# Kernel optimization log

Measured on AMD Instinct MI355X. Metric: run time of the kernel, lower is better.

## Reference

```python
import jax, jax.numpy as jnp
import numpy as np

N = 100_000      # total nodes
E = 1_600_000    # directed edges (before self loops)
G = 1024         # graphs in batch
HEADS, HID, EMB, NCLS = 4, 32, 32, 2
SLOPE = 0.2      # GATConv leaky_relu negative slope
BN_EPS = 1e-5


def setup_inputs() -> dict:
    key = jax.random.key(0)
    ks = jax.random.split(key, 20)
    s = 0.1
    return {
        "x": jax.random.normal(ks[0], (N, 2), jnp.float32),
        "edge_index": jax.random.randint(ks[1], (2, E), 0, N, dtype=jnp.int32),
        "batch": jnp.sort(jax.random.randint(ks[2], (N,), 0, G, dtype=jnp.int32)),
        "W1": jax.random.normal(ks[3], (2, HEADS * HID), jnp.float32) * s,
        "as1": jax.random.normal(ks[4], (HEADS, HID), jnp.float32) * s,
        "ad1": jax.random.normal(ks[5], (HEADS, HID), jnp.float32) * s,
        "b1": jnp.zeros((HEADS * HID,), jnp.float32),
        "g1": jnp.ones((HEADS * HID,), jnp.float32),
        "be1": jnp.zeros((HEADS * HID,), jnp.float32),
        # --- GAT layer 2: 128 -> 32, 1 head, no concat ---
        "W2": jax.random.normal(ks[6], (HEADS * HID, EMB), jnp.float32) * s,
        "as2": jax.random.normal(ks[7], (1, EMB), jnp.float32) * s,
        "ad2": jax.random.normal(ks[8], (1, EMB), jnp.float32) * s,
        "b2": jnp.zeros((EMB,), jnp.float32),
        "g2": jnp.ones((EMB,), jnp.float32),
        "be2": jnp.zeros((EMB,), jnp.float32),
        # --- classifier ---
        "Wc": jax.random.normal(ks[9], (EMB, NCLS), jnp.float32) * s,
        "bc": jnp.zeros((NCLS,), jnp.float32),
    }


def gat_conv(x, src, dst, W, a_src, a_dst, bias, concat):
    """PyG-style GATConv (self loops already appended to src/dst)."""
    n = x.shape[0]
    heads, out = a_src.shape
    h = (x @ W).reshape(n, heads, out)                     # [N,H,D]
    al_src = jnp.sum(h * a_src[None], -1)                  # [N,H]
    al_dst = jnp.sum(h * a_dst[None], -1)                  # [N,H]
    e = jax.nn.leaky_relu(al_src[src] + al_dst[dst], SLOPE)  # [E',H]
    # segment softmax over edges sharing a destination (self loops guarantee coverage)
    m = jax.ops.segment_max(e, dst, num_segments=n)
    e = jnp.exp(e - m[dst])
    z = jax.ops.segment_sum(e, dst, num_segments=n)
    alpha = e / (z[dst] + 1e-16)                           # [E',H]
    msg = h[src] * alpha[:, :, None]                       # [E',H,D]
    out_nodes = jax.ops.segment_sum(msg, dst, num_segments=n)  # [N,H,D]
    if concat:
        return out_nodes.reshape(n, heads * out) + bias
    return out_nodes.mean(1) + bias


def batch_norm(x, gamma, beta):
    mu = x.mean(0)
    var = x.var(0)
    return (x - mu) * jax.lax.rsqrt(var + BN_EPS) * gamma + beta


def reference(x, edge_index, batch, W1, as1, ad1, b1, g1, be1,
              W2, as2, ad2, b2, g2, be2, Wc, bc):
    n = x.shape[0]
    loop = jnp.arange(n, dtype=edge_index.dtype)
    src = jnp.concatenate([edge_index[0], loop])
    dst = jnp.concatenate([edge_index[1], loop])

    h = gat_conv(x, src, dst, W1, as1, ad1, b1, concat=True)
    h = jax.nn.elu(batch_norm(h, g1, be1))     # dropout: eval mode (identity)
    h = gat_conv(h, src, dst, W2, as2, ad2, b2, concat=False)
    h = jax.nn.elu(batch_norm(h, g2, be2))

    # global mean pool per graph
    sums = jax.ops.segment_sum(h, batch, num_segments=G)
    cnt = jax.ops.segment_sum(jnp.ones((n,), h.dtype), batch, num_segments=G)
    emb = sums / jnp.maximum(cnt, 1.0)[:, None]            # [G,EMB]
    return emb @ Wc + bc                                   # [G,2]
```

## Files before the change

kernel.cpp:

```cpp
#include <hip/hip_runtime.h>
#include <hip/hip_bf16.h>
#include <math.h>

#define HEADS 4
#define HID 32
#define EMB 32
#define SLOPE 0.2f
#define BN_EPS 1e-5f
#define STATS_BLOCKS 256
#define MB 128
#define BNUM 256
#define P 256

typedef __attribute__((ext_vector_type(8))) short short8;
typedef __attribute__((ext_vector_type(4))) float fx4;

__device__ __forceinline__ float lrelu(float x) { return x > 0.f ? x : SLOPE * x; }
__device__ __forceinline__ float elu(float x) { return x > 0.f ? x : expm1f(x); }

__device__ __forceinline__ unsigned f2bf_pack(float a, float b) {
    unsigned ua = __float_as_uint(a);
    unsigned ub = __float_as_uint(b);
    unsigned ra = (ua + 0x7fffu + ((ua >> 16) & 1u)) >> 16;
    unsigned rb = (ub + 0x7fffu + ((ub >> 16) & 1u)) >> 16;
    return ra | (rb << 16);
}
__device__ __forceinline__ float bf_lo(unsigned p) { return __uint_as_float(p << 16); }
__device__ __forceinline__ float bf_hi(unsigned p) { return __uint_as_float(p & 0xffff0000u); }

union BfFrag { unsigned u[4]; short8 v; };

__global__ void k_prep(const float* __restrict__ W1, const float* __restrict__ as1,
                       const float* __restrict__ ad1, float* __restrict__ MsMd) {
    int t = threadIdx.x;
    if (t >= 16) return;
    int r = (t >> 2) & 1, h = t & 3;
    const float* a = (t >= 8) ? ad1 : as1;
    float s = 0.f;
#pragma unroll
    for (int d = 0; d < 32; d++) s += W1[r * 128 + h * 32 + d] * a[h * 32 + d];
    MsMd[t] = s;
}

__global__ void __launch_bounds__(256) k_hist(const int* __restrict__ ei,
                                              int* __restrict__ ghist, int E_, int CH) {
    __shared__ int h[BNUM];
    int t = threadIdx.x, p = blockIdx.x;
    h[t] = 0;
    __syncthreads();
    int beg = p * CH, end = beg + CH;
    if (end > E_) end = E_;
    for (int e = beg + t; e < end; e += 256) atomicAdd(&h[ei[E_ + e] >> 9], 1);
    __syncthreads();
    ghist[p * BNUM + t] = h[t];
}

__global__ void __launch_bounds__(1024) k_gscan(const int* __restrict__ ghist,
                                                int* __restrict__ goff, int* __restrict__ sbase,
                                                int* __restrict__ rp, int N_, int E_) {
    __shared__ int s[1024];
    int t = threadIdx.x;
    const int PER = (BNUM * P) / 1024;
    int b0 = t >> 2;
    int p0 = (t & 3) * PER;
    int v[PER];
    int sum = 0;
#pragma unroll
    for (int k = 0; k < PER; k++) {
        v[k] = ghist[(p0 + k) * BNUM + b0];
        sum += v[k];
    }
    s[t] = sum;
    __syncthreads();
    for (int off = 1; off < 1024; off <<= 1) {
        int a = (t >= off) ? s[t - off] : 0;
        __syncthreads();
        s[t] += a;
        __syncthreads();
    }
    int run = s[t] - sum;
#pragma unroll
    for (int k = 0; k < PER; k++) {
        if (p0 + k == 0) sbase[b0] = run;
        goff[(p0 + k) * BNUM + b0] = run;
        run += v[k];
    }
    if (t == 0) {
        sbase[BNUM] = E_;
        rp[N_] = E_ + N_;
    }
}

__global__ void __launch_bounds__(256) k_scatter3(const int* __restrict__ ei,
                                                  const int* __restrict__ goff,
                                                  unsigned* __restrict__ staged,
                                                  int E_, int CH) {
    __shared__ int loff[BNUM];
    __shared__ int lpos[BNUM];
    int t = threadIdx.x, p = blockIdx.x;
    loff[t] = goff[p * BNUM + t];
    lpos[t] = 0;
    __syncthreads();
    int beg = p * CH, end = beg + CH;
    if (end > E_) end = E_;
    for (int e = beg + t; e < end; e += 256) {
        int s = ei[e], d = ei[E_ + e];
        int b = d >> 9;
        unsigned pk = ((unsigned)s << 9) | (unsigned)(d & 511);
        int pos = loff[b] + atomicAdd(&lpos[b], 1);
        staged[pos] = pk;
    }
}

__global__ void __launch_bounds__(512) k_bucket(const unsigned* __restrict__ staged,
                                                const int* __restrict__ sbase,
                                                int* __restrict__ rp, int* __restrict__ esrc,
                                                int N_) {
    int b = blockIdx.x;
    int n0 = b << 9;
    int nn = N_ - n0;
    if (nn > 512) nn = 512;
    if (nn <= 0) return;
    __shared__ int lc[512];
    __shared__ int sc[512];
    __shared__ int wpos[512];
    int t = threadIdx.x;
    lc[t] = 0;
    __syncthreads();
    int sb = sbase[b];
    int m = sbase[b + 1] - sb;
    int eb = sb + (b << 9);
    for (int i = t; i < m; i += 512) atomicAdd(&lc[staged[sb + i] & 511], 1);
    __syncthreads();
    sc[t] = lc[t];
    __syncthreads();
    for (int off = 1; off < 512; off <<= 1) {
        int a = (t >= off) ? sc[t - off] : 0;
        __syncthreads();
        sc[t] += a;
        __syncthreads();
    }
    if (t < nn) {
        int r = eb + (sc[t] - lc[t]) + t;
        rp[n0 + t] = r;
        wpos[t] = r;
        esrc[r + lc[t]] = n0 + t;
    }
    __syncthreads();
    for (int i = t; i < m; i += 512) {
        unsigned p = staged[sb + i];
        int q = atomicAdd(&wpos[p & 511], 1);
        esrc[q] = (int)(p >> 9);
    }
}

__global__ void __launch_bounds__(256) k_agg1f(
        const float* __restrict__ x, const int* __restrict__ rp,
        const int* __restrict__ esrc, const float* __restrict__ MsMd,
        float* __restrict__ nsum, int n) {
    __shared__ float sM[16];
    int t = threadIdx.x;
    if (t < 16) sM[t] = MsMd[t];
    __syncthreads();
    int node = blockIdx.x * 64 + (t >> 2);
    int h = t & 3;
    if (node >= n) return;
    int beg = rp[node], end = rp[node + 1];
    const float2 xd = *reinterpret_cast<const float2*>(&x[(size_t)node * 2]);
    float ald = xd.x * sM[8 + h] + xd.y * sM[12 + h];
    float ms0 = sM[h], ms1 = sM[4 + h];
    float z = 0.f, sx = 0.f, sy = 0.f;
#pragma unroll 2
    for (int e = beg; e < end; e++) {
        int s = esrc[e];
        float2 xs = *reinterpret_cast<const float2*>(&x[(size_t)s * 2]);
        float al = xs.x * ms0 + xs.y * ms1;
        float w = __expf(lrelu(al + ald));
        z += w;
        sx = fmaf(w, xs.x, sx);
        sy = fmaf(w, xs.y, sy);
    }
    float inv = 1.f / (z + 1e-16f);
    nsum[(size_t)node * 8 + h] = sx * inv;
    nsum[(size_t)node * 8 + 4 + h] = sy * inv;
}

__global__ void __launch_bounds__(256) k_mstats(const float* __restrict__ nsum,
                                                float* __restrict__ mpart, int n) {
    int t = threadIdx.x;
    float m[20];
#pragma unroll
    for (int j = 0; j < 20; j++) m[j] = 0.f;
    for (int node = blockIdx.x * 256 + t; node < n; node += gridDim.x * 256) {
        float4 a = *reinterpret_cast<const float4*>(&nsum[(size_t)node * 8]);
        float4 b = *reinterpret_cast<const float4*>(&nsum[(size_t)node * 8 + 4]);
        m[0] += a.x; m[1] += b.x; m[2] += a.x * a.x; m[3] += b.x * b.x; m[4] += a.x * b.x;
        m[5] += a.y; m[6] += b.y; m[7] += a.y * a.y; m[8] += b.y * b.y; m[9] += a.y * b.y;
        m[10] += a.z; m[11] += b.z; m[12] += a.z * a.z; m[13] += b.z * b.z; m[14] += a.z * b.z;
        m[15] += a.w; m[16] += b.w; m[17] += a.w * a.w; m[18] += b.w * b.w; m[19] += a.w * b.w;
    }
#pragma unroll
    for (int off = 1; off < 64; off <<= 1)
#pragma unroll
        for (int j = 0; j < 20; j++) m[j] += __shfl_xor(m[j], off);
    __shared__ float ls[4][20];
    if ((t & 63) == 0)
#pragma unroll
        for (int j = 0; j < 20; j++) ls[t >> 6][j] = m[j];
    __syncthreads();
    if (t < 20) mpart[blockIdx.x * 20 + t] = ls[0][t] + ls[1][t] + ls[2][t] + ls[3][t];
}

__global__ void k_bn1fin(const float* __restrict__ mpart, const float* __restrict__ W1,
                         const float* __restrict__ b1, const float* __restrict__ g1,
                         const float* __restrict__ be1, float4* __restrict__ PQR,
                         int n, int nb) {
    int c = threadIdx.x;
    if (c >= 128) return;
    int h = c >> 5;
    float mx = 0.f, my = 0.f, mxx = 0.f, myy = 0.f, mxy = 0.f;
    for (int b = 0; b < nb; b++) {
        const float* p = &mpart[b * 20 + h * 5];
        mx += p[0]; my += p[1]; mxx += p[2]; myy += p[3]; mxy += p[4];
    }
    float invn = 1.f / (float)n;
    mx *= invn; my *= invn; mxx *= invn; myy *= invn; mxy *= invn;
    float w0 = W1[c], w1 = W1[128 + c], bb = b1[c];
    float mu = w0 * mx + w1 * my + bb;
    float ex2 = w0 * w0 * mxx + w1 * w1 * myy + 2.f * w0 * w1 * mxy
              + 2.f * bb * (w0 * mx + w1 * my) + bb * bb;
    float var = ex2 - mu * mu;
    float A = g1[c] * rsqrtf(var + BN_EPS);
    float B = be1[c] - mu * A;
    PQR[c] = make_float4(A * w0, A * w1, A * bb + B, 0.f);
}

__global__ void __launch_bounds__(256) k_node2m(
        const float* __restrict__ nsum, const float4* __restrict__ PQR,
        const float* __restrict__ W2, const float* __restrict__ as2,
        const float* __restrict__ ad2, unsigned* __restrict__ h2bf,
        float* __restrict__ als2, float* __restrict__ ald2, int n) {
    int t = threadIdx.x;
    int wave = t >> 6, lane = t & 63;
    int col = lane & 15;
    int kgrp = lane >> 4;
    int nb = blockIdx.x * 64 + wave * 16;
    if (nb >= n) return;
    int nodeA = nb + col;
    float4 sx4 = make_float4(0.f, 0.f, 0.f, 0.f), sy4 = sx4;
    if (nodeA < n) {
        sx4 = *reinterpret_cast<const float4*>(&nsum[(size_t)nodeA * 8]);
        sy4 = *reinterpret_cast<const float4*>(&nsum[(size_t)nodeA * 8 + 4]);
    }
    BfFrag b1f[4], b2f[4];
#pragma unroll
    for (int kblk = 0; kblk < 4; kblk++) {
#pragma unroll
        for (int j = 0; j < 8; j += 2) {
            int k = kblk * 32 + kgrp * 8 + j;
            b1f[kblk].u[j >> 1] = f2bf_pack(W2[k * 32 + col], W2[(k + 1) * 32 + col]);
            b2f[kblk].u[j >> 1] = f2bf_pack(W2[k * 32 + 16 + col], W2[(k + 1) * 32 + 16 + col]);
        }
    }
    fx4 acc1 = {0.f, 0.f, 0.f, 0.f};
    fx4 acc2 = {0.f, 0.f, 0.f, 0.f};
    float sxh, syh;
#pragma unroll
    for (int kblk = 0; kblk < 4; kblk++) {
        if (kblk == 0) { sxh = sx4.x; syh = sy4.x; }
        else if (kblk == 1) { sxh = sx4.y; syh = sy4.y; }
        else if (kblk == 2) { sxh = sx4.z; syh = sy4.z; }
        else { sxh = sx4.w; syh = sy4.w; }
        BfFrag af;
        float yk[8];
#pragma unroll
        for (int j = 0; j < 8; j++) {
            int k = kblk * 32 + kgrp * 8 + j;
            float4 pqr = PQR[k];
            yk[j] = elu(fmaf(pqr.x, sxh, fmaf(pqr.y, syh, pqr.z)));
        }
#pragma unroll
        for (int j = 0; j < 8; j += 2) af.u[j >> 1] = f2bf_pack(yk[j], yk[j + 1]);
        acc1 = __builtin_amdgcn_mfma_f32_16x16x32_bf16(af.v, b1f[kblk].v, acc1, 0, 0, 0);
        acc2 = __builtin_amdgcn_mfma_f32_16x16x32_bf16(af.v, b2f[kblk].v, acc2, 0, 0, 0);
    }
    float a2c = as2[col], a2c2 = as2[16 + col];
    float d2c = ad2[col], d2c2 = ad2[16 + col];
#pragma unroll
    for (int r = 0; r < 4; r++) {
        int node = nb + kgrp * 4 + r;
        float v1 = acc1[r], v2 = acc2[r];
        float pS = v1 * a2c + v2 * a2c2;
        float pD = v1 * d2c + v2 * d2c2;
#pragma unroll
        for (int off = 1; off < 16; off <<= 1) {
            pS += __shfl_xor(pS, off);
            pD += __shfl_xor(pD, off);
        }
        float v1n = __shfl_xor(v1, 1);
        float v2n = __shfl_xor(v2, 1);
        if (node < n) {
            if ((col & 1) == 0) {
                h2bf[(size_t)node * 16 + (col >> 1)] = f2bf_pack(v1, v1n);
                h2bf[(size_t)node * 16 + 8 + (col >> 1)] = f2bf_pack(v2, v2n);
            }
            if (col == 0) { als2[node] = pS; ald2[node] = pD; }
        }
    }
}

__global__ void k_stats(const float* __restrict__ x, float* __restrict__ partials,
                        int n, int C) {
    int t = threadIdx.x;
    int G4 = C >> 2;
    int c4 = t & (G4 - 1);
    int rr = t / G4;
    int RPB = 256 / G4;
    float sx = 0.f, sy = 0.f, sz = 0.f, sw_ = 0.f;
    float qx = 0.f, qy = 0.f, qz = 0.f, qw = 0.f;
    for (int r = blockIdx.x * RPB + rr; r < n; r += gridDim.x * RPB) {
        float4 v = *reinterpret_cast<const float4*>(&x[(size_t)r * C + 4 * c4]);
        sx += v.x; sy += v.y; sz += v.z; sw_ += v.w;
        qx += v.x * v.x; qy += v.y * v.y; qz += v.z * v.z; qw += v.w * v.w;
    }
    __shared__ float4 ls[256], ls2[256];
    ls[t] = make_float4(sx, sy, sz, sw_);
    ls2[t] = make_float4(qx, qy, qz, qw);
    __syncthreads();
    if (rr == 0) {
        for (int j = 1; j < RPB; j++) {
            float4 a = ls[j * G4 + c4], b = ls2[j * G4 + c4];
            sx += a.x; sy += a.y; sz += a.z; sw_ += a.w;
            qx += b.x; qy += b.y; qz += b.z; qw += b.w;
        }
        *reinterpret_cast<float4*>(&partials[(size_t)blockIdx.x * 2 * C + 4 * c4]) =
            make_float4(sx, sy, sz, sw_);
        *reinterpret_cast<float4*>(&partials[(size_t)blockIdx.x * 2 * C + C + 4 * c4]) =
            make_float4(qx, qy, qz, qw);
    }
}
__global__ void k_stats2(const float* __restrict__ partials, const float* __restrict__ gamma,
                         const float* __restrict__ beta, float* __restrict__ AB,
                         int n, int C, int nb) {
    __shared__ float ls[512], ls2[512];
    int t = threadIdx.x;
    int R = 512 / C;
    int c = t & (C - 1);
    int r = t / C;
    float s = 0.f, s2 = 0.f;
    for (int b = r; b < nb; b += R) {
        s += partials[(size_t)b * 2 * C + c];
        s2 += partials[(size_t)b * 2 * C + C + c];
    }
    ls[t] = s;
    ls2[t] = s2;
    __syncthreads();
    for (int step = R >> 1; step > 0; step >>= 1) {
        if (r < step) {
            ls[t] += ls[t + step * C];
            ls2[t] += ls2[t + step * C];
        }
        __syncthreads();
    }
    if (r == 0) {
        float mu = ls[t] / n;
        float var = ls2[t] / n - mu * mu;
        float inv = rsqrtf(var + BN_EPS);
        float A = gamma[c] * inv;
        AB[c] = A;
        AB[C + c] = beta[c] - mu * A;
    }
}

__global__ void __launch_bounds__(256) k_agg2(
        const unsigned* __restrict__ h2bf, const float* __restrict__ als2,
        const float* __restrict__ ald2, const int* __restrict__ rp,
        const int* __restrict__ esrc, const float* __restrict__ b2,
        float* __restrict__ out, int n) {
    __shared__ int ss2[4][8][9];
    __shared__ float swv[4][8][9];
    int wslot = threadIdx.x >> 6;
    int lane = threadIdx.x & 63;
    int g = lane >> 3;
    int e = lane & 7;
    int wid = blockIdx.x * 32 + wslot * 8 + g;
    if (wid >= n) return;
    int beg = rp[wid], end = rp[wid + 1];
    float ad = ald2[wid];
    float a0 = 0.f, a1 = 0.f, a2 = 0.f, a3 = 0.f;
    float z = 0.f;
    const uint2* __restrict__ hrow = reinterpret_cast<const uint2*>(h2bf);
    for (int cb = beg; cb < end; cb += 8) {
        int cnt = end - cb;
        if (cnt > 8) cnt = 8;
        if (e < cnt) {
            int s = esrc[cb + e];
            ss2[wslot][g][e] = s;
            swv[wslot][g][e] = __expf(lrelu(als2[s] + ad));
        }
        int j = 0;
        for (; j + 4 <= cnt; j += 4) {
            int s0 = ss2[wslot][g][j];
            int s1 = ss2[wslot][g][j + 1];
            int s2 = ss2[wslot][g][j + 2];
            int s3 = ss2[wslot][g][j + 3];
            float w0 = swv[wslot][g][j];
            float w1 = swv[wslot][g][j + 1];
            float w2 = swv[wslot][g][j + 2];
            float w3 = swv[wslot][g][j + 3];
            uint2 p0 = hrow[(size_t)s0 * 8 + e];
            uint2 p1 = hrow[(size_t)s1 * 8 + e];
            uint2 p2 = hrow[(size_t)s2 * 8 + e];
            uint2 p3 = hrow[(size_t)s3 * 8 + e];
            z += w0 + w1 + w2 + w3;
            a0 = fmaf(w0, bf_lo(p0.x), a0); a1 = fmaf(w0, bf_hi(p0.x), a1);
            a2 = fmaf(w0, bf_lo(p0.y), a2); a3 = fmaf(w0, bf_hi(p0.y), a3);
            a0 = fmaf(w1, bf_lo(p1.x), a0); a1 = fmaf(w1, bf_hi(p1.x), a1);
            a2 = fmaf(w1, bf_lo(p1.y), a2); a3 = fmaf(w1, bf_hi(p1.y), a3);
            a0 = fmaf(w2, bf_lo(p2.x), a0); a1 = fmaf(w2, bf_hi(p2.x), a1);
            a2 = fmaf(w2, bf_lo(p2.y), a2); a3 = fmaf(w2, bf_hi(p2.y), a3);
            a0 = fmaf(w3, bf_lo(p3.x), a0); a1 = fmaf(w3, bf_hi(p3.x), a1);
            a2 = fmaf(w3, bf_lo(p3.y), a2); a3 = fmaf(w3, bf_hi(p3.y), a3);
        }
        for (; j < cnt; j++) {
            int s = ss2[wslot][g][j];
            float wgt = swv[wslot][g][j];
            z += wgt;
            uint2 p = hrow[(size_t)s * 8 + e];
            a0 = fmaf(wgt, bf_lo(p.x), a0);
            a1 = fmaf(wgt, bf_hi(p.x), a1);
            a2 = fmaf(wgt, bf_lo(p.y), a2);
            a3 = fmaf(wgt, bf_hi(p.y), a3);
        }
    }
    float inv = 1.f / (z + 1e-16f);
    const float4 bv = *reinterpret_cast<const float4*>(&b2[4 * e]);
    float4 o = make_float4(a0 * inv + bv.x, a1 * inv + bv.y, a2 * inv + bv.z, a3 * inv + bv.w);
    *reinterpret_cast<float4*>(&out[(size_t)wid * 32 + 4 * e]) = o;
}

__global__ void k_pool(const float* __restrict__ x, const float* __restrict__ AB2,
                       const int* __restrict__ batch, const float* __restrict__ Wc,
                       const float* __restrict__ bc, float* __restrict__ out, int n, int G_) {
    int wid = (blockIdx.x * blockDim.x + threadIdx.x) >> 6;
    int lane = threadIdx.x & 63;
    if (wid >= G_) return;
    int lo = 0, hi = n;
    while (lo < hi) {
        int mid = (lo + hi) >> 1;
        if (batch[mid] < wid) lo = mid + 1; else hi = mid;
    }
    int beg = lo;
    hi = n;
    while (lo < hi) {
        int mid = (lo + hi) >> 1;
        if (batch[mid] < wid + 1) lo = mid + 1; else hi = mid;
    }
    int end = lo;
    int half = lane >> 5, f = lane & 31;
    float A = AB2[f], B = AB2[32 + f];
    float acc = 0.f;
    for (int r = beg + half; r < end; r += 2) {
        float v = x[(size_t)r * 32 + f] * A + B;
        acc += elu(v);
    }
    acc += __shfl_xor(acc, 32);
    float cntf = (float)((end - beg) > 1 ? (end - beg) : 1);
    float embv = acc / cntf;
    float p0 = embv * Wc[f * 2], p1 = embv * Wc[f * 2 + 1];
#pragma unroll
    for (int o = 1; o < 32; o <<= 1) {
        p0 += __shfl_xor(p0, o);
        p1 += __shfl_xor(p1, o);
    }
    if (lane == 0) {
        out[wid * 2] = p0 + bc[0];
        out[wid * 2 + 1] = p1 + bc[1];
    }
}

extern "C" void kernel_launch(void* const* d_in, const int* in_sizes, int n_in,
                              void* d_out, int out_size, void* d_ws, size_t ws_size,
                              hipStream_t stream) {
    const float* x = (const float*)d_in[0];
    const int* ei = (const int*)d_in[1];
    const int* batch = (const int*)d_in[2];
    const float* W1 = (const float*)d_in[3];
    const float* as1 = (const float*)d_in[4];
    const float* ad1 = (const float*)d_in[5];
    const float* b1 = (const float*)d_in[6];
    const float* g1 = (const float*)d_in[7];
    const float* be1 = (const float*)d_in[8];
    const float* W2 = (const float*)d_in[9];
    const float* as2 = (const float*)d_in[10];
    const float* ad2 = (const float*)d_in[11];
    const float* b2 = (const float*)d_in[12];
    const float* g2 = (const float*)d_in[13];
    const float* be2 = (const float*)d_in[14];
    const float* Wc = (const float*)d_in[15];
    const float* bc = (const float*)d_in[16];
    float* out = (float*)d_out;

    const int N = in_sizes[0] / 2;
    const int E = in_sizes[1] / 2;
    const int G = out_size / 2;
    const int Etot = E + N;
    const int B = (N + 511) >> 9;
    const int CH = (E + P - 1) / P;

    char* w = (char*)d_ws;
    size_t off = 0;
    auto alloc = [&](size_t bytes) { void* p = w + off; off = (off + bytes + 255) & ~(size_t)255; return p; };
    float* nsum = (float*)alloc((size_t)N * 8 * 4);
    unsigned* l2buf = (unsigned*)alloc((size_t)N * 50 * 4);
    int* esrc = (int*)alloc((size_t)Etot * 4);
    unsigned* staged = (unsigned*)alloc((size_t)E * 4);
    int* rp = (int*)alloc((size_t)(N + 1) * 4);
    int* ghist = (int*)alloc((size_t)P * BNUM * 4);
    int* goff = (int*)alloc((size_t)P * BNUM * 4);
    int* sbase = (int*)alloc((BNUM + 1) * 4);
    float* partials = (float*)alloc((size_t)STATS_BLOCKS * 256 * 4);
    float* mpart = (float*)alloc((size_t)MB * 20 * 4);
    float* AB2 = (float*)alloc(64 * 4);
    float* MsMd = (float*)alloc(64 * 4);
    float4* PQR = (float4*)alloc(128 * 16);
    unsigned* h2bf = l2buf;
    float* als2 = (float*)(l2buf + (size_t)N * 16);
    float* ald2 = (float*)(l2buf + (size_t)N * 17);
    float* out2 = (float*)(l2buf + (size_t)N * 18);

    k_prep<<<1, 64, 0, stream>>>(W1, as1, ad1, MsMd);
    k_hist<<<P, 256, 0, stream>>>(ei, ghist, E, CH);
    k_gscan<<<1, 1024, 0, stream>>>(ghist, goff, sbase, rp, N, E);
    k_scatter3<<<P, 256, 0, stream>>>(ei, goff, staged, E, CH);
    k_bucket<<<B, 512, 0, stream>>>(staged, sbase, rp, esrc, N);
    k_agg1f<<<(N + 63) / 64, 256, 0, stream>>>(x, rp, esrc, MsMd, nsum, N);
    k_mstats<<<MB, 256, 0, stream>>>(nsum, mpart, N);
    k_bn1fin<<<1, 128, 0, stream>>>(mpart, W1, b1, g1, be1, PQR, N, MB);
    k_node2m<<<(N + 63) / 64, 256, 0, stream>>>(nsum, PQR, W2, as2, ad2, h2bf, als2, ald2, N);
    k_agg2<<<(N + 31) / 32, 256, 0, stream>>>(h2bf, als2, ald2, rp, esrc, b2, out2, N);
    k_stats<<<STATS_BLOCKS, 256, 0, stream>>>(out2, partials, N, 32);
    k_stats2<<<1, 512, 0, stream>>>(partials, g2, be2, AB2, N, 32, STATS_BLOCKS);
    k_pool<<<(G * 64 + 255) / 256, 256, 0, stream>>>(out2, AB2, batch, Wc, bc, out, N, G);
}
```

Baseline: 203.4 us.

## Fuse batch-norm statistics reductions into both aggregation kernels

Layer-1 moment accumulation moves into k_agg1f and layer-2 sum/sum-of-squares moves into k_agg2, so the separate k_mstats and k_stats kernels go away. This saves two launches and two full re-reads of the node feature arrays. The cost is that the final reducers (k_bn1fin, k_stats2) now sum over many more per-block partials (about 1563 and 3125 instead of 128 and 256). k_agg2 also gains extra shared memory and a tree reduction with several __syncthreads, which may hurt occupancy.

Result: slower. 233.1 us (+14.6%).

```diff
diff --git a/kernel.cpp b/kernel.cpp
--- a/kernel.cpp
+++ b/kernel.cpp
@@ -7,8 +7,6 @@
 #define EMB 32
 #define SLOPE 0.2f
 #define BN_EPS 1e-5f
-#define STATS_BLOCKS 256
-#define MB 128
 #define BNUM 256
 #define P 256
 
@@ -157,82 +155,98 @@
 __global__ void __launch_bounds__(256) k_agg1f(
         const float* __restrict__ x, const int* __restrict__ rp,
         const int* __restrict__ esrc, const float* __restrict__ MsMd,
-        float* __restrict__ nsum, int n) {
+        float* __restrict__ nsum, float* __restrict__ mpart, int n) {
     __shared__ float sM[16];
+    __shared__ float lsm[4][4][5];
     int t = threadIdx.x;
     if (t < 16) sM[t] = MsMd[t];
     __syncthreads();
     int node = blockIdx.x * 64 + (t >> 2);
     int h = t & 3;
-    if (node >= n) return;
-    int beg = rp[node], end = rp[node + 1];
-    const float2 xd = *reinterpret_cast<const float2*>(&x[(size_t)node * 2]);
-    float ald = xd.x * sM[8 + h] + xd.y * sM[12 + h];
-    float ms0 = sM[h], ms1 = sM[4 + h];
-    float z = 0.f, sx = 0.f, sy = 0.f;
+    float sxv = 0.f, syv = 0.f;
+    if (node < n) {
+        int beg = rp[node], end = rp[node + 1];
+        const float2 xd = *reinterpret_cast<const float2*>(&x[(size_t)node * 2]);
+        float ald = xd.x * sM[8 + h] + xd.y * sM[12 + h];
+        float ms0 = sM[h], ms1 = sM[4 + h];
+        float z = 0.f, sx = 0.f, sy = 0.f;
 #pragma unroll 2
-    for (int e = beg; e < end; e++) {
-        int s = esrc[e];
-        float2 xs = *reinterpret_cast<const float2*>(&x[(size_t)s * 2]);
-        float al = xs.x * ms0 + xs.y * ms1;
-        float w = __expf(lrelu(al + ald));
-        z += w;
-        sx = fmaf(w, xs.x, sx);
-        sy = fmaf(w, xs.y, sy);
-    }
-    float inv = 1.f / (z + 1e-16f);
-    nsum[(size_t)node * 8 + h] = sx * inv;
-    nsum[(size_t)node * 8 + 4 + h] = sy * inv;
-}
-
-__global__ void __launch_bounds__(256) k_mstats(const float* __restrict__ nsum,
-                                                float* __restrict__ mpart, int n) {
-    int t = threadIdx.x;
-    float m[20];
-#pragma unroll
-    for (int j = 0; j < 20; j++) m[j] = 0.f;
-    for (int node = blockIdx.x * 256 + t; node < n; node += gridDim.x * 256) {
-        float4 a = *reinterpret_cast<const float4*>(&nsum[(size_t)node * 8]);
-        float4 b = *reinterpret_cast<const float4*>(&nsum[(size_t)node * 8 + 4]);
-        m[0] += a.x; m[1] += b.x; m[2] += a.x * a.x; m[3] += b.x * b.x; m[4] += a.x * b.x;
-        m[5] += a.y; m[6] += b.y; m[7] += a.y * a.y; m[8] += b.y * b.y; m[9] += a.y * b.y;
-        m[10] += a.z; m[11] += b.z; m[12] += a.z * a.z; m[13] += b.z * b.z; m[14] += a.z * b.z;
-        m[15] += a.w; m[16] += b.w; m[17] += a.w * a.w; m[18] += b.w * b.w; m[19] += a.w * b.w;
-    }
-#pragma unroll
-    for (int off = 1; off < 64; off <<= 1)
-#pragma unroll
-        for (int j = 0; j < 20; j++) m[j] += __shfl_xor(m[j], off);
-    __shared__ float ls[4][20];
-    if ((t & 63) == 0)
-#pragma unroll
-        for (int j = 0; j < 20; j++) ls[t >> 6][j] = m[j];
-    __syncthreads();
-    if (t < 20) mpart[blockIdx.x * 20 + t] = ls[0][t] + ls[1][t] + ls[2][t] + ls[3][t];
-}
-
-__global__ void k_bn1fin(const float* __restrict__ mpart, const float* __restrict__ W1,
-                         const float* __restrict__ b1, const float* __restrict__ g1,
-                         const float* __restrict__ be1, float4* __restrict__ PQR,
-                         int n, int nb) {
-    int c = threadIdx.x;
-    if (c >= 128) return;
-    int h = c >> 5;
-    float mx = 0.f, my = 0.f, mxx = 0.f, myy = 0.f, mxy = 0.f;
-    for (int b = 0; b < nb; b++) {
-        const float* p = &mpart[b * 20 + h * 5];
-        mx += p[0]; my += p[1]; mxx += p[2]; myy += p[3]; mxy += p[4];
-    }
-    float invn = 1.f / (float)n;
-    mx *= invn; my *= invn; mxx *= invn; myy *= invn; mxy *= invn;
-    float w0 = W1[c], w1 = W1[128 + c], bb = b1[c];
-    float mu = w0 * mx + w1 * my + bb;
-    float ex2 = w0 * w0 * mxx + w1 * w1 * myy + 2.f * w0 * w1 * mxy
-              + 2.f * bb * (w0 * mx + w1 * my) + bb * bb;
-    float var = ex2 - mu * mu;
-    float A = g1[c] * rsqrtf(var + BN_EPS);
-    float B = be1[c] - mu * A;
-    PQR[c] = make_float4(A * w0, A * w1, A * bb + B, 0.f);
+        for (int e = beg; e < end; e++) {
+            int s = esrc[e];
+            float2 xs = *reinterpret_cast<const float2*>(&x[(size_t)s * 2]);
+            float al = xs.x * ms0 + xs.y * ms1;
+            float w = __expf(lrelu(al + ald));
+            z += w;
+            sx = fmaf(w, xs.x, sx);
+            sy = fmaf(w, xs.y, sy);
+        }
+        float inv = 1.f / (z + 1e-16f);
+        sxv = sx * inv;
+        syv = sy * inv;
+        nsum[(size_t)node * 8 + h] = sxv;
+        nsum[(size_t)node * 8 + 4 + h] = syv;
+    }
+    float m0 = sxv, m1 = syv, m2 = sxv * sxv, m3 = syv * syv, m4 = sxv * syv;
+#pragma unroll
+    for (int off = 4; off < 64; off <<= 1) {
+        m0 += __shfl_xor(m0, off);
+        m1 += __shfl_xor(m1, off);
+        m2 += __shfl_xor(m2, off);
+        m3 += __shfl_xor(m3, off);
+        m4 += __shfl_xor(m4, off);
+    }
+    int lane = t & 63, wave = t >> 6;
+    if (lane < 4) {
+        lsm[wave][lane][0] = m0;
+        lsm[wave][lane][1] = m1;
+        lsm[wave][lane][2] = m2;
+        lsm[wave][lane][3] = m3;
+        lsm[wave][lane][4] = m4;
+    }
+    __syncthreads();
+    if (t < 20) {
+        int hh = t / 5, j = t % 5;
+        mpart[(size_t)blockIdx.x * 20 + t] =
+            lsm[0][hh][j] + lsm[1][hh][j] + lsm[2][hh][j] + lsm[3][hh][j];
+    }
+}
+
+__global__ void __launch_bounds__(640) k_bn1fin(
+        const float* __restrict__ mpart, const float* __restrict__ W1,
+        const float* __restrict__ b1, const float* __restrict__ g1,
+        const float* __restrict__ be1, float4* __restrict__ PQR, int n, int nb) {
+    __shared__ float ls[20][32];
+    __shared__ float mom[20];
+    int t = threadIdx.x;
+    if (t < 640) {
+        int j = t % 20, r = t / 20;
+        float s = 0.f;
+        for (int b = r; b < nb; b += 32) s += mpart[(size_t)b * 20 + j];
+        ls[j][r] = s;
+    }
+    __syncthreads();
+    if (t < 20) {
+        float s = 0.f;
+#pragma unroll
+        for (int r = 0; r < 32; r++) s += ls[t][r];
+        mom[t] = s;
+    }
+    __syncthreads();
+    if (t < 128) {
+        int c = t, h = c >> 5;
+        float invn = 1.f / (float)n;
+        float mx = mom[h * 5 + 0] * invn, my = mom[h * 5 + 1] * invn;
+        float mxx = mom[h * 5 + 2] * invn, myy = mom[h * 5 + 3] * invn;
+        float mxy = mom[h * 5 + 4] * invn;
+        float w0 = W1[c], w1 = W1[128 + c], bb = b1[c];
+        float mu = w0 * mx + w1 * my + bb;
+        float ex2 = w0 * w0 * mxx + w1 * w1 * myy + 2.f * w0 * w1 * mxy
+                  + 2.f * bb * (w0 * mx + w1 * my) + bb * bb;
+        float var = ex2 - mu * mu;
+        float A = g1[c] * rsqrtf(var + BN_EPS);
+        float B = be1[c] - mu * A;
+        PQR[c] = make_float4(A * w0, A * w1, A * bb + B, 0.f);
+    }
 }
 
 __global__ void __launch_bounds__(256) k_node2m(
@@ -309,36 +323,6 @@
     }
 }
 
-__global__ void k_stats(const float* __restrict__ x, float* __restrict__ partials,
-                        int n, int C) {
-    int t = threadIdx.x;
-    int G4 = C >> 2;
-    int c4 = t & (G4 - 1);
-    int rr = t / G4;
-    int RPB = 256 / G4;
-    float sx = 0.f, sy = 0.f, sz = 0.f, sw_ = 0.f;
-    float qx = 0.f, qy = 0.f, qz = 0.f, qw = 0.f;
-    for (int r = blockIdx.x * RPB + rr; r < n; r += gridDim.x * RPB) {
-        float4 v = *reinterpret_cast<const float4*>(&x[(size_t)r * C + 4 * c4]);
-        sx += v.x; sy += v.y; sz += v.z; sw_ += v.w;
-        qx += v.x * v.x; qy += v.y * v.y; qz += v.z * v.z; qw += v.w * v.w;
-    }
-    __shared__ float4 ls[256], ls2[256];
-    ls[t] = make_float4(sx, sy, sz, sw_);
-    ls2[t] = make_float4(qx, qy, qz, qw);
-    __syncthreads();
-    if (rr == 0) {
-        for (int j = 1; j < RPB; j++) {
-            float4 a = ls[j * G4 + c4], b = ls2[j * G4 + c4];
-            sx += a.x; sy += a.y; sz += a.z; sw_ += a.w;
-            qx += b.x; qy += b.y; qz += b.z; qw += b.w;
-        }
-        *reinterpret_cast<float4*>(&partials[(size_t)blockIdx.x * 2 * C + 4 * c4]) =
-            make_float4(sx, sy, sz, sw_);
-        *reinterpret_cast<float4*>(&partials[(size_t)blockIdx.x * 2 * C + C + 4 * c4]) =
-            make_float4(qx, qy, qz, qw);
-    }
-}
 __global__ void k_stats2(const float* __restrict__ partials, const float* __restrict__ gamma,
                          const float* __restrict__ beta, float* __restrict__ AB,
                          int n, int C, int nb) {
@@ -376,67 +360,93 @@
         const unsigned* __restrict__ h2bf, const float* __restrict__ als2,
         const float* __restrict__ ald2, const int* __restrict__ rp,
         const int* __restrict__ esrc, const float* __restrict__ b2,
-        float* __restrict__ out, int n) {
+        float* __restrict__ out, float* __restrict__ partials, int n) {
     __shared__ int ss2[4][8][9];
     __shared__ float swv[4][8][9];
+    __shared__ float red[8][33][4];
+    __shared__ float red2[8][33][4];
     int wslot = threadIdx.x >> 6;
     int lane = threadIdx.x & 63;
     int g = lane >> 3;
     int e = lane & 7;
     int wid = blockIdx.x * 32 + wslot * 8 + g;
-    if (wid >= n) return;
-    int beg = rp[wid], end = rp[wid + 1];
-    float ad = ald2[wid];
-    float a0 = 0.f, a1 = 0.f, a2 = 0.f, a3 = 0.f;
-    float z = 0.f;
-    const uint2* __restrict__ hrow = reinterpret_cast<const uint2*>(h2bf);
-    for (int cb = beg; cb < end; cb += 8) {
-        int cnt = end - cb;
-        if (cnt > 8) cnt = 8;
-        if (e < cnt) {
-            int s = esrc[cb + e];
-            ss2[wslot][g][e] = s;
-            swv[wslot][g][e] = __expf(lrelu(als2[s] + ad));
-        }
-        int j = 0;
-        for (; j + 4 <= cnt; j += 4) {
-            int s0 = ss2[wslot][g][j];
-            int s1 = ss2[wslot][g][j + 1];
-            int s2 = ss2[wslot][g][j + 2];
-            int s3 = ss2[wslot][g][j + 3];
-            float w0 = swv[wslot][g][j];
-            float w1 = swv[wslot][g][j + 1];
-            float w2 = swv[wslot][g][j + 2];
-            float w3 = swv[wslot][g][j + 3];
-            uint2 p0 = hrow[(size_t)s0 * 8 + e];
-            uint2 p1 = hrow[(size_t)s1 * 8 + e];
-            uint2 p2 = hrow[(size_t)s2 * 8 + e];
-            uint2 p3 = hrow[(size_t)s3 * 8 + e];
-            z += w0 + w1 + w2 + w3;
-            a0 = fmaf(w0, bf_lo(p0.x), a0); a1 = fmaf(w0, bf_hi(p0.x), a1);
-            a2 = fmaf(w0, bf_lo(p0.y), a2); a3 = fmaf(w0, bf_hi(p0.y), a3);
-            a0 = fmaf(w1, bf_lo(p1.x), a0); a1 = fmaf(w1, bf_hi(p1.x), a1);
-            a2 = fmaf(w1, bf_lo(p1.y), a2); a3 = fmaf(w1, bf_hi(p1.y), a3);
-            a0 = fmaf(w2, bf_lo(p2.x), a0); a1 = fmaf(w2, bf_hi(p2.x), a1);
-            a2 = fmaf(w2, bf_lo(p2.y), a2); a3 = fmaf(w2, bf_hi(p2.y), a3);
-            a0 = fmaf(w3, bf_lo(p3.x), a0); a1 = fmaf(w3, bf_hi(p3.x), a1);
-            a2 = fmaf(w3, bf_lo(p3.y), a2); a3 = fmaf(w3, bf_hi(p3.y), a3);
-        }
-        for (; j < cnt; j++) {
-            int s = ss2[wslot][g][j];
-            float wgt = swv[wslot][g][j];
-            z += wgt;
-            uint2 p = hrow[(size_t)s * 8 + e];
-            a0 = fmaf(wgt, bf_lo(p.x), a0);
-            a1 = fmaf(wgt, bf_hi(p.x), a1);
-            a2 = fmaf(wgt, bf_lo(p.y), a2);
-            a3 = fmaf(wgt, bf_hi(p.y), a3);
-        }
-    }
-    float inv = 1.f / (z + 1e-16f);
-    const float4 bv = *reinterpret_cast<const float4*>(&b2[4 * e]);
-    float4 o = make_float4(a0 * inv + bv.x, a1 * inv + bv.y, a2 * inv + bv.z, a3 * inv + bv.w);
-    *reinterpret_cast<float4*>(&out[(size_t)wid * 32 + 4 * e]) = o;
+    float4 o = make_float4(0.f, 0.f, 0.f, 0.f);
+    if (wid < n) {
+        int beg = rp[wid], end = rp[wid + 1];
+        float ad = ald2[wid];
+        float a0 = 0.f, a1 = 0.f, a2 = 0.f, a3 = 0.f;
+        float z = 0.f;
+        const uint2* __restrict__ hrow = reinterpret_cast<const uint2*>(h2bf);
+        for (int cb = beg; cb < end; cb += 8) {
+            int cnt = end - cb;
+            if (cnt > 8) cnt = 8;
+            if (e < cnt) {
+                int s = esrc[cb + e];
+                ss2[wslot][g][e] = s;
+                swv[wslot][g][e] = __expf(lrelu(als2[s] + ad));
+            }
+            int j = 0;
+            for (; j + 4 <= cnt; j += 4) {
+                int s0 = ss2[wslot][g][j];
+                int s1 = ss2[wslot][g][j + 1];
+                int s2 = ss2[wslot][g][j + 2];
+                int s3 = ss2[wslot][g][j + 3];
+                float w0 = swv[wslot][g][j];
+                float w1 = swv[wslot][g][j + 1];
+                float w2 = swv[wslot][g][j + 2];
+                float w3 = swv[wslot][g][j + 3];
+                uint2 p0 = hrow[(size_t)s0 * 8 + e];
+                uint2 p1 = hrow[(size_t)s1 * 8 + e];
+                uint2 p2 = hrow[(size_t)s2 * 8 + e];
+                uint2 p3 = hrow[(size_t)s3 * 8 + e];
+                z += w0 + w1 + w2 + w3;
+                a0 = fmaf(w0, bf_lo(p0.x), a0); a1 = fmaf(w0, bf_hi(p0.x), a1);
+                a2 = fmaf(w0, bf_lo(p0.y), a2); a3 = fmaf(w0, bf_hi(p0.y), a3);
+                a0 = fmaf(w1, bf_lo(p1.x), a0); a1 = fmaf(w1, bf_hi(p1.x), a1);
+                a2 = fmaf(w1, bf_lo(p1.y), a2); a3 = fmaf(w1, bf_hi(p1.y), a3);
+                a0 = fmaf(w2, bf_lo(p2.x), a0); a1 = fmaf(w2, bf_hi(p2.x), a1);
+                a2 = fmaf(w2, bf_lo(p2.y), a2); a3 = fmaf(w2, bf_hi(p2.y), a3);
+                a0 = fmaf(w3, bf_lo(p3.x), a0); a1 = fmaf(w3, bf_hi(p3.x), a1);
+                a2 = fmaf(w3, bf_lo(p3.y), a2); a3 = fmaf(w3, bf_hi(p3.y), a3);
+            }
+            for (; j < cnt; j++) {
+                int s = ss2[wslot][g][j];
+                float wgt = swv[wslot][g][j];
+                z += wgt;
+                uint2 p = hrow[(size_t)s * 8 + e];
+                a0 = fmaf(wgt, bf_lo(p.x), a0);
+                a1 = fmaf(wgt, bf_hi(p.x), a1);
+                a2 = fmaf(wgt, bf_lo(p.y), a2);
+                a3 = fmaf(wgt, bf_hi(p.y), a3);
+            }
+        }
+        float inv = 1.f / (z + 1e-16f);
+        const float4 bv = *reinterpret_cast<const float4*>(&b2[4 * e]);
+        o = make_float4(a0 * inv + bv.x, a1 * inv + bv.y, a2 * inv + bv.z, a3 * inv + bv.w);
+        *reinterpret_cast<float4*>(&out[(size_t)wid * 32 + 4 * e]) = o;
+    }
+    int ns = wslot * 8 + g;
+    red[e][ns][0] = o.x; red[e][ns][1] = o.y; red[e][ns][2] = o.z; red[e][ns][3] = o.w;
+    red2[e][ns][0] = o.x * o.x; red2[e][ns][1] = o.y * o.y;
+    red2[e][ns][2] = o.z * o.z; red2[e][ns][3] = o.w * o.w;
+    __syncthreads();
+    for (int step = 16; step > 0; step >>= 1) {
+        if (ns < step) {
+#pragma unroll
+            for (int i = 0; i < 4; i++) {
+                red[e][ns][i] += red[e][ns + step][i];
+                red2[e][ns][i] += red2[e][ns + step][i];
+            }
+        }
+        __syncthreads();
+    }
+    if (ns == 0) {
+#pragma unroll
+        for (int i = 0; i < 4; i++) {
+            partials[(size_t)blockIdx.x * 64 + 4 * e + i] = red[e][0][i];
+            partials[(size_t)blockIdx.x * 64 + 32 + 4 * e + i] = red2[e][0][i];
+        }
+    }
 }
 
 __global__ void k_pool(const float* __restrict__ x, const float* __restrict__ AB2,
@@ -507,6 +517,8 @@
     const int Etot = E + N;
     const int B = (N + 511) >> 9;
     const int CH = (E + P - 1) / P;
+    const int NB1 = (N + 63) / 64;
+    const int NB2 = (N + 31) / 32;
 
     char* w = (char*)d_ws;
     size_t off = 0;
@@ -519,8 +531,8 @@
     int* ghist = (int*)alloc((size_t)P * BNUM * 4);
     int* goff = (int*)alloc((size_t)P * BNUM * 4);
     int* sbase = (int*)alloc((BNUM + 1) * 4);
-    float* partials = (float*)alloc((size_t)STATS_BLOCKS * 256 * 4);
-    float* mpart = (float*)alloc((size_t)MB * 20 * 4);
+    float* partials = (float*)alloc((size_t)NB2 * 64 * 4);
+    float* mpart = (float*)alloc((size_t)NB1 * 20 * 4);
     float* AB2 = (float*)alloc(64 * 4);
     float* MsMd = (float*)alloc(64 * 4);
     float4* PQR = (float4*)alloc(128 * 16);
@@ -534,12 +546,10 @@
     k_gscan<<<1, 1024, 0, stream>>>(ghist, goff, sbase, rp, N, E);
     k_scatter3<<<P, 256, 0, stream>>>(ei, goff, staged, E, CH);
     k_bucket<<<B, 512, 0, stream>>>(staged, sbase, rp, esrc, N);
-    k_agg1f<<<(N + 63) / 64, 256, 0, stream>>>(x, rp, esrc, MsMd, nsum, N);
-    k_mstats<<<MB, 256, 0, stream>>>(nsum, mpart, N);
-    k_bn1fin<<<1, 128, 0, stream>>>(mpart, W1, b1, g1, be1, PQR, N, MB);
+    k_agg1f<<<NB1, 256, 0, stream>>>(x, rp, esrc, MsMd, nsum, mpart, N);
+    k_bn1fin<<<1, 640, 0, stream>>>(mpart, W1, b1, g1, be1, PQR, N, NB1);
     k_node2m<<<(N + 63) / 64, 256, 0, stream>>>(nsum, PQR, W2, as2, ad2, h2bf, als2, ald2, N);
-    k_agg2<<<(N + 31) / 32, 256, 0, stream>>>(h2bf, als2, ald2, rp, esrc, b2, out2, N);
-    k_stats<<<STATS_BLOCKS, 256, 0, stream>>>(out2, partials, N, 32);
-    k_stats2<<<1, 512, 0, stream>>>(partials, g2, be2, AB2, N, 32, STATS_BLOCKS);
+    k_agg2<<<NB2, 256, 0, stream>>>(h2bf, als2, ald2, rp, esrc, b2, out2, partials, N);
+    k_stats2<<<1, 512, 0, stream>>>(partials, g2, be2, AB2, N, 32, NB2);
     k_pool<<<(G * 64 + 255) / 256, 256, 0, stream>>>(out2, AB2, batch, Wc, bc, out, N, G);
 }
```
